# Optimization experiments

Measured on AMD Instinct MI355X. Metric: run time of the kernel, lower is better.

## Reference

```python
import jax, jax.numpy as jnp
import numpy as np

N, E, D, H, C = 40000, 640000, 128, 4, 32  # nodes, edges, in_hid, heads, out_channels/head
NUM_NODE_TYPE, NUM_EDGE_TYPE = 8, 8
NEG_SLOPE = 0.2
EDGE_TYPE_SELF = 0


def setup_inputs() -> dict:
    key = jax.random.key(0)
    ks = jax.random.split(key, 12)
    x = jax.random.normal(ks[0], (N, D), dtype=jnp.float32)
    # build edges with no self-loops (the module filters src==dst before adding self-loops)
    src = jax.random.randint(ks[1], (E,), 0, N, dtype=jnp.int32)
    off = jax.random.randint(ks[2], (E,), 1, N, dtype=jnp.int32)
    dst = (src + off) % N
    edge_index = jnp.stack([src, dst])  # [2, E]
    node_type = jax.random.randint(ks[3], (N,), 0, NUM_NODE_TYPE, dtype=jnp.int32)
    edge_type = jax.random.randint(ks[4], (E,), 0, NUM_EDGE_TYPE, dtype=jnp.int32)
    g = 0.05
    Wq = jax.random.normal(ks[5], (H * C, D), dtype=jnp.float32) * g
    Wk = jax.random.normal(ks[6], (H * C, D), dtype=jnp.float32) * g
    Wv = jax.random.normal(ks[7], (H * C, D), dtype=jnp.float32) * g
    att_i = jax.random.normal(ks[8], (1, H, C), dtype=jnp.float32) * g
    att_j = jax.random.normal(ks[9], (1, H, C), dtype=jnp.float32) * g
    bias = jnp.zeros((H * C,), dtype=jnp.float32)
    node_emb_table = jax.random.normal(ks[10], (NUM_NODE_TYPE, D), dtype=jnp.float32) * g
    edge_emb_table = jax.random.normal(ks[11], (NUM_EDGE_TYPE, D), dtype=jnp.float32) * g
    return {"x": x, "edge_index": edge_index, "node_type": node_type,
            "edge_type": edge_type, "Wq": Wq, "Wk": Wk, "Wv": Wv,
            "att_i": att_i, "att_j": att_j, "bias": bias,
            "node_emb_table": node_emb_table, "edge_emb_table": edge_emb_table}


def reference(x, edge_index, node_type, edge_type, Wq, Wk, Wv,
              att_i, att_j, bias, node_emb_table, edge_emb_table):
    n = x.shape[0]
    # node-type embedding add
    x = x + node_emb_table[node_type]                       # [N, D]
    xq = x @ Wq.T                                           # [N, H*C]
    # add self-loops (input edges contain no src==dst by construction)
    self_idx = jnp.arange(n, dtype=edge_index.dtype)
    src = jnp.concatenate([edge_index[0], self_idx])        # [E+N]
    dst = jnp.concatenate([edge_index[1], self_idx])        # [E+N]
    et = jnp.concatenate([edge_type,
                          jnp.full((n,), EDGE_TYPE_SELF, dtype=edge_type.dtype)])
    edge_emb = edge_emb_table[et]                           # [E+N, D]
    # message: per-edge gather + K/V linear + additive attention
    x_j = x[src] + edge_emb                                 # [E+N, D]
    xq_i = xq[dst].reshape(-1, H, C)                        # [E+N, H, C]
    x_k = (x_j @ Wk.T).reshape(-1, H, C)
    x_v = (x_j @ Wv.T).reshape(-1, H, C)
    alpha = (xq_i * att_i).sum(-1) + (x_k * att_j).sum(-1)  # [E+N, H]
    alpha = jax.nn.leaky_relu(alpha, NEG_SLOPE)
    # segment softmax over destination nodes (PyG softmax, eps=1e-16)
    amax = jax.ops.segment_max(alpha, dst, num_segments=n)  # [N, H]
    alpha = jnp.exp(alpha - amax[dst])
    denom = jax.ops.segment_sum(alpha, dst, num_segments=n)
    alpha = alpha / (denom[dst] + 1e-16)
    # scatter-add weighted values
    out = jax.ops.segment_sum(x_v * alpha[..., None], dst, num_segments=n)  # [N, H, C]
    return out.reshape(n, H * C) + bias
```

## Files before the change

### kernel.cpp

```cpp
#include <hip/hip_runtime.h>
#include <math.h>

#define NN 40000
#define NE 640000
#define D 128
#define NH 4
#define NC 32
#define NEG 0.2f

typedef __attribute__((ext_vector_type(8))) short bf16x8;
typedef __attribute__((ext_vector_type(4))) float f32x4;

__device__ __forceinline__ unsigned pack_bf16(float a, float b) {
  unsigned ua = __float_as_uint(a), ub = __float_as_uint(b);
  ua = (ua + 0x7FFFu + ((ua >> 16) & 1u)) >> 16;
  ub = (ub + 0x7FFFu + ((ub >> 16) & 1u)) & 0xFFFF0000u;
  return ub | ua;
}

__device__ __forceinline__ bf16x8 to_bf16x8(float4 a, float4 b) {
  union { bf16x8 v; unsigned u[4]; } r;
  r.u[0] = pack_bf16(a.x, a.y);
  r.u[1] = pack_bf16(a.z, a.w);
  r.u[2] = pack_bf16(b.x, b.y);
  r.u[3] = pack_bf16(b.z, b.w);
  return r.v;
}

__device__ __forceinline__ float4 f4add(float4 a, float4 b) {
  return make_float4(a.x + b.x, a.y + b.y, a.z + b.z, a.w + b.w);
}

__global__ __launch_bounds__(256) void k_tables(
    const float* __restrict__ Wq, const float* __restrict__ Wk,
    const float* __restrict__ Wv,
    const float* __restrict__ att_i, const float* __restrict__ att_j,
    const float* __restrict__ eemb,
    float* __restrict__ ev, float* __restrict__ a_et,
    unsigned* __restrict__ Wvh, int* __restrict__ counts) {
  __shared__ float sm[1024];
  int b = blockIdx.x, t = threadIdx.x;
  if (b == 0) {
    for (int j = t; j < 1024; j += 256) {
      int isq = (j < 512);
      int h = (j >> 7) & 3, d = j & 127;
      const float* __restrict__ Wm = isq ? Wq : Wk;
      const float* __restrict__ am = isq ? att_i : att_j;
      float s = 0.f;
#pragma unroll
      for (int c = 0; c < NC; ++c) s = fmaf(am[h * NC + c], Wm[(h * NC + c) * D + d], s);
      sm[j] = s;
    }
    __syncthreads();
    for (int j = t; j < 1024; j += 256) {
      int r = j >> 6;
      int c2 = (j & 63) * 2;
      float a = 0.f, bb = 0.f;
      if (r < 8) { a = sm[r * 128 + c2]; bb = sm[r * 128 + c2 + 1]; }
      Wvh[(128 + r) * 64 + (j & 63)] = pack_bf16(a, bb);
    }
    if (t < 32) {
      int ty = t >> 2, hh = t & 3;
      const float* wrow = sm + 512 + hh * 128;
      const float* __restrict__ emb = eemb + ty * D;
      float s = 0.f;
#pragma unroll 8
      for (int d = 0; d < D; ++d) s = fmaf(wrow[d], emb[d], s);
      a_et[t] = s;
    }
  } else if (b <= 8) {
    int ty = b - 1;
    if (t < 128) sm[t] = eemb[ty * D + t];
    __syncthreads();
    if (t < 128) {
      const float4* __restrict__ wr = (const float4*)(Wv + (size_t)t * D);
      const float4* __restrict__ er = (const float4*)sm;
      float s = 0.f;
#pragma unroll
      for (int k = 0; k < 32; ++k) {
        float4 ww = wr[k], ee = er[k];
        s = fmaf(ww.x, ee.x, s); s = fmaf(ww.y, ee.y, s);
        s = fmaf(ww.z, ee.z, s); s = fmaf(ww.w, ee.w, s);
      }
      ev[ty * D + t] = s;
    }
  } else if (b <= 16) {
    int j0 = (b - 9) * 1024;
    for (int j = j0 + t; j < j0 + 1024; j += 256)
      Wvh[j] = pack_bf16(Wv[2 * j], Wv[2 * j + 1]);
  } else {
    int i = (b - 17) * 256 + t;
    if (i < NN / 4) ((int4*)counts)[i] = make_int4(0, 0, 0, 0);
  }
}

__global__ __launch_bounds__(256) void k_sxi(
    const int* __restrict__ ei, const int* __restrict__ etype,
    int* __restrict__ counts, unsigned* __restrict__ packed,
    const float* __restrict__ x, const int* __restrict__ node_type,
    const float* __restrict__ nemb, const unsigned* __restrict__ Wvh,
    unsigned* __restrict__ xvh, float* __restrict__ aq, float* __restrict__ ak) {
  int b = blockIdx.x, t = threadIdx.x;
  if (b % 5 != 0) {
    int sb = b - (b + 4) / 5;
    int i = sb * 256 + t;
    int src = ei[i];
    int dst = ei[NE + i];
    int et  = etype[i];
    int r = atomicAdd(&counts[dst], 1);
    if (r < 63) packed[(dst << 6) + r] = (unsigned)src | ((unsigned)et << 16);
    return;
  }
  int bb = b / 5;
  int w = t >> 6, l = t & 63;
  int quad = l >> 4, col = l & 15;
  int n0w = bb * 64 + w * 16;
  int node = n0w + col;
  int ntA = node_type[node];
  const float4* __restrict__ xr = (const float4*)(x + (size_t)node * D);
  const float4* __restrict__ nr = (const float4*)(nemb + (size_t)ntA * D);
  bf16x8 afr[4];
#pragma unroll
  for (int s = 0; s < 4; ++s) {
    const float4* p = xr + s * 8 + quad * 2;
    const float4* q4 = nr + s * 8 + quad * 2;
    afr[s] = to_bf16x8(f4add(p[0], q4[0]), f4add(p[1], q4[1]));
  }
  f32x4 acc[9];
#pragma unroll
  for (int ct = 0; ct < 9; ++ct) acc[ct] = (f32x4){0.f, 0.f, 0.f, 0.f};
#pragma unroll
  for (int ct = 0; ct < 9; ++ct) {
    const unsigned* __restrict__ brow = Wvh + (size_t)(ct * 16 + col) * 64;
#pragma unroll
    for (int s = 0; s < 4; ++s) {
      bf16x8 bfr = *(const bf16x8*)(brow + s * 16 + quad * 4);
      acc[ct] = __builtin_amdgcn_mfma_f32_16x16x32_bf16(afr[s], bfr, acc[ct], 0, 0, 0);
    }
  }
  int nodes[4];
#pragma unroll
  for (int r = 0; r < 4; ++r) nodes[r] = n0w + quad * 4 + r;
#pragma unroll
  for (int ct = 0; ct < 8; ++ct) {
#pragma unroll
    for (int r = 0; r < 4; ++r) {
      float val = acc[ct][r];
      float pv = __shfl_xor(val, 1);
      if (!(col & 1)) {
        xvh[nodes[r] * 64 + ct * 8 + (col >> 1)] = pack_bf16(val, pv);
      }
    }
  }
  if (col < 4) {
#pragma unroll
    for (int r = 0; r < 4; ++r) aq[nodes[r] * NH + col] = acc[8][r];
  } else if (col < 8) {
#pragma unroll
    for (int r = 0; r < 4; ++r) ak[nodes[r] * NH + (col - 4)] = acc[8][r];
  }
}

__global__ __launch_bounds__(256) void k_gather(const int* __restrict__ counts,
        const unsigned* __restrict__ packed,
        const float* __restrict__ aq, const float* __restrict__ ak,
        const float* __restrict__ a_et, const unsigned* __restrict__ xvh,
        const float* __restrict__ ev, const float* __restrict__ bias,
        float* __restrict__ out) {
  int n = (int)((blockIdx.x * blockDim.x + threadIdx.x) >> 6);
  int l = threadIdx.x & 63;
  if (n >= NN) return;
  int g = l >> 3, q = l & 7;
  int h = q >> 1;
  float aqh = aq[n * NH + h];
  int e0 = n << 6;
  int deg = min(counts[n], 63);
  int m = deg + 1;
  const uint4* __restrict__ xv4 = (const uint4*)xvh;
  float acc[16];
#pragma unroll
  for (int k = 0; k < 16; ++k) acc[k] = 0.f;
  float ps[8];
#pragma unroll
  for (int k = 0; k < 8; ++k) ps[k] = 0.f;
  int iters = (m + 7) >> 3;
  int i = g;
  bool val = (i < m);
  unsigned rec = (val && i < deg) ? packed[e0 + i] : (unsigned)n;
  int src = (int)(rec & 0xFFFFu), etc = (int)(rec >> 16);
  float sA = ak[src * NH + h] + a_et[etc * NH + h];
  uint4 vb0 = xv4[src * 16 + 2 * q];
  uint4 vb1 = xv4[src * 16 + 2 * q + 1];
  for (int it = 0; it < iters; ++it) {
    int i2 = i + 8;
    bool v2 = (i2 < m);
    float sAn = 0.f; int etn = 0;
    uint4 vb0n = make_uint4(0, 0, 0, 0), vb1n = make_uint4(0, 0, 0, 0);
    if (it + 1 < iters) {
      unsigned rec2 = (v2 && i2 < deg) ? packed[e0 + i2] : (unsigned)n;
      int s2 = (int)(rec2 & 0xFFFFu);
      etn = (int)(rec2 >> 16);
      sAn = ak[s2 * NH + h] + a_et[etn * NH + h];
      vb0n = xv4[s2 * 16 + 2 * q];
      vb1n = xv4[s2 * 16 + 2 * q + 1];
    }
    float s = aqh + sA;
    s = (s > 0.f) ? s : NEG * s;
    float p = val ? __expf(s) : 0.f;
#pragma unroll
    for (int tt = 0; tt < 8; ++tt) ps[tt] += (etc == tt) ? p : 0.f;
    float f[16];
    f[0]  = __uint_as_float(vb0.x << 16); f[1]  = __uint_as_float(vb0.x & 0xFFFF0000u);
    f[2]  = __uint_as_float(vb0.y << 16); f[3]  = __uint_as_float(vb0.y & 0xFFFF0000u);
    f[4]  = __uint_as_float(vb0.z << 16); f[5]  = __uint_as_float(vb0.z & 0xFFFF0000u);
    f[6]  = __uint_as_float(vb0.w << 16); f[7]  = __uint_as_float(vb0.w & 0xFFFF0000u);
    f[8]  = __uint_as_float(vb1.x << 16); f[9]  = __uint_as_float(vb1.x & 0xFFFF0000u);
    f[10] = __uint_as_float(vb1.y << 16); f[11] = __uint_as_float(vb1.y & 0xFFFF0000u);
    f[12] = __uint_as_float(vb1.z << 16); f[13] = __uint_as_float(vb1.z & 0xFFFF0000u);
    f[14] = __uint_as_float(vb1.w << 16); f[15] = __uint_as_float(vb1.w & 0xFFFF0000u);
#pragma unroll
    for (int k = 0; k < 16; ++k) acc[k] = fmaf(p, f[k], acc[k]);
    i = i2; val = v2; sA = sAn; etc = etn; vb0 = vb0n; vb1 = vb1n;
  }
#pragma unroll
  for (int tt = 0; tt < 8; ++tt) {
    ps[tt] += __shfl_xor(ps[tt], 8);
    ps[tt] += __shfl_xor(ps[tt], 16);
    ps[tt] += __shfl_xor(ps[tt], 32);
  }
  float dsum = ((ps[0] + ps[1]) + (ps[2] + ps[3])) + ((ps[4] + ps[5]) + (ps[6] + ps[7]));
  float psg = ps[0];
#pragma unroll
  for (int tt = 1; tt < 8; ++tt) psg = (g == tt) ? ps[tt] : psg;
  const float4* __restrict__ ep = (const float4*)(ev + g * D + 16 * q);
  float4 ea0 = ep[0], ea1 = ep[1], ea2 = ep[2], ea3 = ep[3];
  acc[0]  = fmaf(psg, ea0.x, acc[0]);
  acc[1]  = fmaf(psg, ea0.y, acc[1]);
  acc[2]  = fmaf(psg, ea0.z, acc[2]);
  acc[3]  = fmaf(psg, ea0.w, acc[3]);
  acc[4]  = fmaf(psg, ea1.x, acc[4]);
  acc[5]  = fmaf(psg, ea1.y, acc[5]);
  acc[6]  = fmaf(psg, ea1.z, acc[6]);
  acc[7]  = fmaf(psg, ea1.w, acc[7]);
  acc[8]  = fmaf(psg, ea2.x, acc[8]);
  acc[9]  = fmaf(psg, ea2.y, acc[9]);
  acc[10] = fmaf(psg, ea2.z, acc[10]);
  acc[11] = fmaf(psg, ea2.w, acc[11]);
  acc[12] = fmaf(psg, ea3.x, acc[12]);
  acc[13] = fmaf(psg, ea3.y, acc[13]);
  acc[14] = fmaf(psg, ea3.z, acc[14]);
  acc[15] = fmaf(psg, ea3.w, acc[15]);
#pragma unroll
  for (int k = 0; k < 16; ++k) {
    acc[k] += __shfl_xor(acc[k], 8);
    acc[k] += __shfl_xor(acc[k], 16);
    acc[k] += __shfl_xor(acc[k], 32);
  }
  if (g == 0) {
    float inv = 1.f / (dsum + 1e-16f);
    const float4* __restrict__ b4 = (const float4*)(bias + 16 * q);
    float4* __restrict__ op = (float4*)(out + (size_t)n * D + 16 * q);
#pragma unroll
    for (int k4 = 0; k4 < 4; ++k4) {
      float4 bb = b4[k4];
      op[k4] = make_float4(acc[4 * k4 + 0] * inv + bb.x,
                           acc[4 * k4 + 1] * inv + bb.y,
                           acc[4 * k4 + 2] * inv + bb.z,
                           acc[4 * k4 + 3] * inv + bb.w);
    }
  }
}

extern "C" void kernel_launch(void* const* d_in, const int* in_sizes, int n_in,
                              void* d_out, int out_size, void* d_ws, size_t ws_size,
                              hipStream_t stream) {
  const float* x      = (const float*)d_in[0];
  const int*   ei     = (const int*)d_in[1];
  const int*   ntype  = (const int*)d_in[2];
  const int*   etype  = (const int*)d_in[3];
  const float* Wq     = (const float*)d_in[4];
  const float* Wk     = (const float*)d_in[5];
  const float* Wv     = (const float*)d_in[6];
  const float* att_i  = (const float*)d_in[7];
  const float* att_j  = (const float*)d_in[8];
  const float* bias   = (const float*)d_in[9];
  const float* nemb   = (const float*)d_in[10];
  const float* eemb   = (const float*)d_in[11];
  float* out = (float*)d_out;

  float* ws     = (float*)d_ws;
  unsigned* xvh = (unsigned*)ws;
  float* aq     = ws + (size_t)NN * 64;
  float* ak     = aq + NN * NH;
  float* ev     = ak + NN * NH;
  float* a_et   = ev + 1024;
  unsigned* Wvh = (unsigned*)(a_et + 32);
  int*   counts = (int*)(Wvh + 9216);
  unsigned* packed = (unsigned*)(counts + NN);

  k_tables<<<dim3(64), dim3(256), 0, stream>>>(Wq, Wk, Wv, att_i, att_j, eemb,
                                               ev, a_et, Wvh, counts);
  k_sxi<<<dim3(3125), dim3(256), 0, stream>>>(ei, etype, counts, packed,
                                              x, ntype, nemb, Wvh, xvh, aq, ak);
  k_gather<<<dim3((NN + 3) / 4), dim3(256), 0, stream>>>(counts, packed, aq, ak, a_et,
                                                         xvh, ev, bias, out);
}
```

Baseline: 175.8 us.

## Split per-node edge counters into 8 banks to reduce atomic contention

The edge-binning atomic counter per destination node is split into 8 sub-counters selected by block index. Each bank gets its own 16-slot region in a 128-slot-per-node packed buffer, and the stores become nontemporal. The gather kernel reads all 8 counts, builds prefix offsets and maps each edge index to a bank slot through a chain of compares. This aims to cut same-address atomic serialization, at the cost of 8x counter zeroing, a buffer twice as large, and extra index arithmetic in gather. It also caps each bank at 16 edges, which could drop edges if one bank fills for a node.

```diff
diff --git a/kernel.cpp b/kernel.cpp
--- a/kernel.cpp
+++ b/kernel.cpp
@@ -37,7 +37,7 @@
     const float* __restrict__ att_i, const float* __restrict__ att_j,
     const float* __restrict__ eemb,
     float* __restrict__ ev, float* __restrict__ a_et,
-    unsigned* __restrict__ Wvh, int* __restrict__ counts) {
+    unsigned* __restrict__ Wvh, int* __restrict__ counts8) {
   __shared__ float sm[1024];
   int b = blockIdx.x, t = threadIdx.x;
   if (b == 0) {
@@ -90,13 +90,13 @@
       Wvh[j] = pack_bf16(Wv[2 * j], Wv[2 * j + 1]);
   } else {
     int i = (b - 17) * 256 + t;
-    if (i < NN / 4) ((int4*)counts)[i] = make_int4(0, 0, 0, 0);
+    if (i < NN * 8 / 4) ((int4*)counts8)[i] = make_int4(0, 0, 0, 0);
   }
 }
 
 __global__ __launch_bounds__(256) void k_sxi(
     const int* __restrict__ ei, const int* __restrict__ etype,
-    int* __restrict__ counts, unsigned* __restrict__ packed,
+    int* __restrict__ counts8, unsigned* __restrict__ packed,
     const float* __restrict__ x, const int* __restrict__ node_type,
     const float* __restrict__ nemb, const unsigned* __restrict__ Wvh,
     unsigned* __restrict__ xvh, float* __restrict__ aq, float* __restrict__ ak) {
@@ -104,11 +104,14 @@
   if (b % 5 != 0) {
     int sb = b - (b + 4) / 5;
     int i = sb * 256 + t;
+    int bank = b & 7;
     int src = ei[i];
     int dst = ei[NE + i];
     int et  = etype[i];
-    int r = atomicAdd(&counts[dst], 1);
-    if (r < 63) packed[(dst << 6) + r] = (unsigned)src | ((unsigned)et << 16);
+    int r = atomicAdd(&counts8[dst * 8 + bank], 1);
+    if (r < 16)
+      __builtin_nontemporal_store((unsigned)src | ((unsigned)et << 16),
+                                  &packed[(dst << 7) + (bank << 4) + r]);
     return;
   }
   int bb = b / 5;
@@ -161,7 +164,23 @@
   }
 }
 
-__global__ __launch_bounds__(256) void k_gather(const int* __restrict__ counts,
+__device__ __forceinline__ unsigned fetch_rec(const unsigned* __restrict__ packed,
+    int n, int j, int p1, int p2, int p3, int p4, int p5, int p6, int p7, int p8) {
+  if (j >= p8) return (unsigned)n;
+  int bk = (j >= p1) + (j >= p2) + (j >= p3) + (j >= p4) +
+           (j >= p5) + (j >= p6) + (j >= p7);
+  int pb = 0;
+  pb = (j >= p1) ? p1 : pb;
+  pb = (j >= p2) ? p2 : pb;
+  pb = (j >= p3) ? p3 : pb;
+  pb = (j >= p4) ? p4 : pb;
+  pb = (j >= p5) ? p5 : pb;
+  pb = (j >= p6) ? p6 : pb;
+  pb = (j >= p7) ? p7 : pb;
+  return packed[(n << 7) + (bk << 4) + (j - pb)];
+}
+
+__global__ __launch_bounds__(256) void k_gather(const int* __restrict__ counts8,
         const unsigned* __restrict__ packed,
         const float* __restrict__ aq, const float* __restrict__ ak,
         const float* __restrict__ a_et, const unsigned* __restrict__ xvh,
@@ -173,9 +192,13 @@
   int g = l >> 3, q = l & 7;
   int h = q >> 1;
   float aqh = aq[n * NH + h];
-  int e0 = n << 6;
-  int deg = min(counts[n], 63);
-  int m = deg + 1;
+  const int4* __restrict__ c4 = (const int4*)(counts8 + n * 8);
+  int4 ca = c4[0], cb = c4[1];
+  int d0 = min(ca.x, 16), d1 = min(ca.y, 16), d2 = min(ca.z, 16), d3 = min(ca.w, 16);
+  int d4 = min(cb.x, 16), d5 = min(cb.y, 16), d6 = min(cb.z, 16), d7 = min(cb.w, 16);
+  int p1 = d0, p2 = p1 + d1, p3 = p2 + d2, p4 = p3 + d3;
+  int p5 = p4 + d4, p6 = p5 + d5, p7 = p6 + d6, p8 = p7 + d7;
+  int m = p8 + 1;
   const uint4* __restrict__ xv4 = (const uint4*)xvh;
   float acc[16];
 #pragma unroll
@@ -186,7 +209,7 @@
   int iters = (m + 7) >> 3;
   int i = g;
   bool val = (i < m);
-  unsigned rec = (val && i < deg) ? packed[e0 + i] : (unsigned)n;
+  unsigned rec = fetch_rec(packed, n, i, p1, p2, p3, p4, p5, p6, p7, p8);
   int src = (int)(rec & 0xFFFFu), etc = (int)(rec >> 16);
   float sA = ak[src * NH + h] + a_et[etc * NH + h];
   uint4 vb0 = xv4[src * 16 + 2 * q];
@@ -197,7 +220,7 @@
     float sAn = 0.f; int etn = 0;
     uint4 vb0n = make_uint4(0, 0, 0, 0), vb1n = make_uint4(0, 0, 0, 0);
     if (it + 1 < iters) {
-      unsigned rec2 = (v2 && i2 < deg) ? packed[e0 + i2] : (unsigned)n;
+      unsigned rec2 = fetch_rec(packed, n, i2, p1, p2, p3, p4, p5, p6, p7, p8);
       int s2 = (int)(rec2 & 0xFFFFu);
       etn = (int)(rec2 >> 16);
       sAn = ak[s2 * NH + h] + a_et[etn * NH + h];
@@ -288,20 +311,20 @@
   const float* eemb   = (const float*)d_in[11];
   float* out = (float*)d_out;
 
-  float* ws     = (float*)d_ws;
-  unsigned* xvh = (unsigned*)ws;
-  float* aq     = ws + (size_t)NN * 64;
-  float* ak     = aq + NN * NH;
-  float* ev     = ak + NN * NH;
-  float* a_et   = ev + 1024;
-  unsigned* Wvh = (unsigned*)(a_et + 32);
-  int*   counts = (int*)(Wvh + 9216);
-  unsigned* packed = (unsigned*)(counts + NN);
-
-  k_tables<<<dim3(64), dim3(256), 0, stream>>>(Wq, Wk, Wv, att_i, att_j, eemb,
-                                               ev, a_et, Wvh, counts);
-  k_sxi<<<dim3(3125), dim3(256), 0, stream>>>(ei, etype, counts, packed,
+  float* ws      = (float*)d_ws;
+  unsigned* xvh  = (unsigned*)ws;
+  float* aq      = ws + (size_t)NN * 64;
+  float* ak      = aq + NN * NH;
+  float* ev      = ak + NN * NH;
+  float* a_et    = ev + 1024;
+  unsigned* Wvh  = (unsigned*)(a_et + 32);
+  int* counts8   = (int*)(Wvh + 9216);
+  unsigned* packed = (unsigned*)(counts8 + NN * 8);
+
+  k_tables<<<dim3(330), dim3(256), 0, stream>>>(Wq, Wk, Wv, att_i, att_j, eemb,
+                                                ev, a_et, Wvh, counts8);
+  k_sxi<<<dim3(3125), dim3(256), 0, stream>>>(ei, etype, counts8, packed,
                                               x, ntype, nemb, Wvh, xvh, aq, ak);
-  k_gather<<<dim3((NN + 3) / 4), dim3(256), 0, stream>>>(counts, packed, aq, ak, a_et,
+  k_gather<<<dim3((NN + 3) / 4), dim3(256), 0, stream>>>(counts8, packed, aq, ak, a_et,
                                                          xvh, ev, bias, out);
 }
```

After: 178.5 us. About the same (+1.5%).

## Fold weight-table prep into node kernel and replace counts zeroing with memset

Applied to the files above, without the earlier changes.

Removes the separate k_tables launch. Each node block of k_sxi now recomputes the folded att·Wq/att·Wk vectors into shared memory and converts Wv rows to bf16 on the fly. Extra blocks appended to the grid compute the a_et and ev tables. Counts are zeroed with hipMemsetAsync instead of a kernel. This trades one kernel launch for redundant per-block computation of the folded query/key weights, plus fp32 Wv reads and conversions in every node block.

```diff
diff --git a/kernel.cpp b/kernel.cpp
--- a/kernel.cpp
+++ b/kernel.cpp
@@ -31,78 +31,57 @@
   return make_float4(a.x + b.x, a.y + b.y, a.z + b.z, a.w + b.w);
 }
 
-__global__ __launch_bounds__(256) void k_tables(
-    const float* __restrict__ Wq, const float* __restrict__ Wk,
-    const float* __restrict__ Wv,
-    const float* __restrict__ att_i, const float* __restrict__ att_j,
-    const float* __restrict__ eemb,
-    float* __restrict__ ev, float* __restrict__ a_et,
-    unsigned* __restrict__ Wvh, int* __restrict__ counts) {
-  __shared__ float sm[1024];
-  int b = blockIdx.x, t = threadIdx.x;
-  if (b == 0) {
-    for (int j = t; j < 1024; j += 256) {
-      int isq = (j < 512);
-      int h = (j >> 7) & 3, d = j & 127;
-      const float* __restrict__ Wm = isq ? Wq : Wk;
-      const float* __restrict__ am = isq ? att_i : att_j;
-      float s = 0.f;
-#pragma unroll
-      for (int c = 0; c < NC; ++c) s = fmaf(am[h * NC + c], Wm[(h * NC + c) * D + d], s);
-      sm[j] = s;
-    }
-    __syncthreads();
-    for (int j = t; j < 1024; j += 256) {
-      int r = j >> 6;
-      int c2 = (j & 63) * 2;
-      float a = 0.f, bb = 0.f;
-      if (r < 8) { a = sm[r * 128 + c2]; bb = sm[r * 128 + c2 + 1]; }
-      Wvh[(128 + r) * 64 + (j & 63)] = pack_bf16(a, bb);
-    }
-    if (t < 32) {
-      int ty = t >> 2, hh = t & 3;
-      const float* wrow = sm + 512 + hh * 128;
-      const float* __restrict__ emb = eemb + ty * D;
-      float s = 0.f;
-#pragma unroll 8
-      for (int d = 0; d < D; ++d) s = fmaf(wrow[d], emb[d], s);
-      a_et[t] = s;
-    }
-  } else if (b <= 8) {
-    int ty = b - 1;
-    if (t < 128) sm[t] = eemb[ty * D + t];
-    __syncthreads();
-    if (t < 128) {
-      const float4* __restrict__ wr = (const float4*)(Wv + (size_t)t * D);
-      const float4* __restrict__ er = (const float4*)sm;
-      float s = 0.f;
-#pragma unroll
-      for (int k = 0; k < 32; ++k) {
-        float4 ww = wr[k], ee = er[k];
-        s = fmaf(ww.x, ee.x, s); s = fmaf(ww.y, ee.y, s);
-        s = fmaf(ww.z, ee.z, s); s = fmaf(ww.w, ee.w, s);
-      }
-      ev[ty * D + t] = s;
-    }
-  } else if (b <= 16) {
-    int j0 = (b - 9) * 1024;
-    for (int j = j0 + t; j < j0 + 1024; j += 256)
-      Wvh[j] = pack_bf16(Wv[2 * j], Wv[2 * j + 1]);
-  } else {
-    int i = (b - 17) * 256 + t;
-    if (i < NN / 4) ((int4*)counts)[i] = make_int4(0, 0, 0, 0);
-  }
-}
-
 __global__ __launch_bounds__(256) void k_sxi(
     const int* __restrict__ ei, const int* __restrict__ etype,
     int* __restrict__ counts, unsigned* __restrict__ packed,
     const float* __restrict__ x, const int* __restrict__ node_type,
-    const float* __restrict__ nemb, const unsigned* __restrict__ Wvh,
+    const float* __restrict__ nemb, const float* __restrict__ eemb,
+    const float* __restrict__ Wq, const float* __restrict__ Wk,
+    const float* __restrict__ Wv,
+    const float* __restrict__ att_i, const float* __restrict__ att_j,
+    float* __restrict__ ev, float* __restrict__ a_et,
     unsigned* __restrict__ xvh, float* __restrict__ aq, float* __restrict__ ak) {
+  __shared__ float sm[1024];
   int b = blockIdx.x, t = threadIdx.x;
+  if (b >= 3125) {
+    int tb = b - 3125;
+    if (tb == 0) {
+      for (int j = t; j < 512; j += 256) {
+        int h = j >> 7, d = j & 127;
+        float s = 0.f;
+#pragma unroll
+        for (int c = 0; c < NC; ++c) s = fmaf(att_j[h * NC + c], Wk[(h * NC + c) * D + d], s);
+        sm[j] = s;
+      }
+      __syncthreads();
+      if (t < 32) {
+        int ty = t >> 2, hh = t & 3;
+        float s = 0.f;
+#pragma unroll 8
+        for (int d = 0; d < D; ++d) s = fmaf(sm[hh * D + d], eemb[ty * D + d], s);
+        a_et[t] = s;
+      }
+    } else {
+      int ty = tb - 1;
+      if (t < 128) sm[t] = eemb[ty * D + t];
+      __syncthreads();
+      if (t < 128) {
+        const float4* __restrict__ wr = (const float4*)(Wv + (size_t)t * D);
+        const float4* __restrict__ er = (const float4*)sm;
+        float s = 0.f;
+#pragma unroll
+        for (int k = 0; k < 32; ++k) {
+          float4 ww = wr[k], ee = er[k];
+          s = fmaf(ww.x, ee.x, s); s = fmaf(ww.y, ee.y, s);
+          s = fmaf(ww.z, ee.z, s); s = fmaf(ww.w, ee.w, s);
+        }
+        ev[ty * D + t] = s;
+      }
+    }
+    return;
+  }
   if (b % 5 != 0) {
-    int sb = b - (b + 4) / 5;
+    int sb = b - b / 5 - 1;
     int i = sb * 256 + t;
     int src = ei[i];
     int dst = ei[NE + i];
@@ -111,6 +90,17 @@
     if (r < 63) packed[(dst << 6) + r] = (unsigned)src | ((unsigned)et << 16);
     return;
   }
+  for (int j = t; j < 1024; j += 256) {
+    int isq = (j < 512);
+    int h = (j >> 7) & 3, d = j & 127;
+    const float* __restrict__ Wm = isq ? Wq : Wk;
+    const float* __restrict__ am = isq ? att_i : att_j;
+    float s = 0.f;
+#pragma unroll
+    for (int c = 0; c < NC; ++c) s = fmaf(am[h * NC + c], Wm[(h * NC + c) * D + d], s);
+    sm[j] = s;
+  }
+  __syncthreads();
   int bb = b / 5;
   int w = t >> 6, l = t & 63;
   int quad = l >> 4, col = l & 15;
@@ -130,12 +120,27 @@
 #pragma unroll
   for (int ct = 0; ct < 9; ++ct) acc[ct] = (f32x4){0.f, 0.f, 0.f, 0.f};
 #pragma unroll
-  for (int ct = 0; ct < 9; ++ct) {
-    const unsigned* __restrict__ brow = Wvh + (size_t)(ct * 16 + col) * 64;
+  for (int ct = 0; ct < 8; ++ct) {
+    const float* __restrict__ brow = Wv + (size_t)(ct * 16 + col) * D;
 #pragma unroll
     for (int s = 0; s < 4; ++s) {
-      bf16x8 bfr = *(const bf16x8*)(brow + s * 16 + quad * 4);
+      const float4* wp = (const float4*)(brow + s * 32 + quad * 8);
+      bf16x8 bfr = to_bf16x8(wp[0], wp[1]);
       acc[ct] = __builtin_amdgcn_mfma_f32_16x16x32_bf16(afr[s], bfr, acc[ct], 0, 0, 0);
+    }
+  }
+  {
+#pragma unroll
+    for (int s = 0; s < 4; ++s) {
+      bf16x8 bfr;
+      if (col < 8) {
+        const float4* wp = (const float4*)&sm[col * D + s * 32 + quad * 8];
+        bfr = to_bf16x8(wp[0], wp[1]);
+      } else {
+        union { bf16x8 v; unsigned u[4]; } z; z.u[0] = z.u[1] = z.u[2] = z.u[3] = 0;
+        bfr = z.v;
+      }
+      acc[8] = __builtin_amdgcn_mfma_f32_16x16x32_bf16(afr[s], bfr, acc[8], 0, 0, 0);
     }
   }
   int nodes[4];
@@ -288,20 +293,20 @@
   const float* eemb   = (const float*)d_in[11];
   float* out = (float*)d_out;
 
-  float* ws     = (float*)d_ws;
-  unsigned* xvh = (unsigned*)ws;
-  float* aq     = ws + (size_t)NN * 64;
-  float* ak     = aq + NN * NH;
-  float* ev     = ak + NN * NH;
-  float* a_et   = ev + 1024;
-  unsigned* Wvh = (unsigned*)(a_et + 32);
-  int*   counts = (int*)(Wvh + 9216);
+  float* ws      = (float*)d_ws;
+  unsigned* xvh  = (unsigned*)ws;
+  float* aq      = ws + (size_t)NN * 64;
+  float* ak      = aq + NN * NH;
+  float* ev      = ak + NN * NH;
+  float* a_et    = ev + 1024;
+  int* counts    = (int*)(a_et + 32);
   unsigned* packed = (unsigned*)(counts + NN);
 
-  k_tables<<<dim3(64), dim3(256), 0, stream>>>(Wq, Wk, Wv, att_i, att_j, eemb,
-                                               ev, a_et, Wvh, counts);
-  k_sxi<<<dim3(3125), dim3(256), 0, stream>>>(ei, etype, counts, packed,
-                                              x, ntype, nemb, Wvh, xvh, aq, ak);
+  hipMemsetAsync(counts, 0, NN * sizeof(int), stream);
+  k_sxi<<<dim3(3134), dim3(256), 0, stream>>>(ei, etype, counts, packed,
+                                              x, ntype, nemb, eemb,
+                                              Wq, Wk, Wv, att_i, att_j,
+                                              ev, a_et, xvh, aq, ak);
   k_gather<<<dim3((NN + 3) / 4), dim3(256), 0, stream>>>(counts, packed, aq, ak, a_et,
                                                          xvh, ev, bias, out);
 }
```

New measurement: 192.9 us. 1.1x slower.
